# Kernel optimization log

Measured on AMD Instinct MI355X. Metric: run time of the kernel, lower is better.

## Reference

```python
import jax, jax.numpy as jnp
import numpy as np

B = 131072   # batch
D = 128      # input_dim
H = 512      # hidden_dim
E = 2        # number of tasks/experts (fixed in module)
O = 2        # output dim (fixed in module)


def setup_inputs() -> dict:
    key = jax.random.key(0)
    k0, k1, k2, k3 = jax.random.split(key, 4)
    x = jax.random.normal(k0, (B, D), jnp.float32)
    # kaiming-uniform-ish scale for weights
    w1 = jax.random.normal(k1, (E, H, D), jnp.float32) * (1.0 / np.sqrt(D).astype(np.float32))
    b1 = jnp.zeros((E, H), jnp.float32)
    w2 = jax.random.normal(k2, (E, O, H), jnp.float32) * (1.0 / np.sqrt(H).astype(np.float32))
    b2 = jnp.zeros((E, O), jnp.float32)
    # buffer is zeros in torch; randomize so routing is non-degenerate
    prototypes = jax.random.normal(k3, (E, D), jnp.float32)
    return {"x": x, "w1": w1, "b1": b1, "w2": w2, "b2": b2, "prototypes": prototypes}


def reference(x, w1, b1, w2, b2, prototypes):
    # Routing: torch.cdist -> argmin. Squared distance has the same argmin
    # as euclidean distance (sqrt is monotone), so skip the sqrt.
    diff = x[:, None, :] - prototypes[None, :, :]          # [B, E, D]
    d2 = jnp.sum(diff * diff, axis=-1)                     # [B, E]
    t = jnp.argmin(d2, axis=1)                             # [B] int

    # Only E=2 experts: evaluate both and select, instead of a per-sample
    # gathered [B,H,D] weight tensor (this replaces the torch python loop).
    h = jax.nn.relu(jnp.einsum('bd,ehd->beh', x, w1) + b1[None])   # [B, E, H]
    out_all = jnp.einsum('beh,eoh->beo', h, w2) + b2[None]          # [B, E, O]
    out = jnp.take_along_axis(out_all, t[:, None, None], axis=1)[:, 0, :]  # [B, O]
    return out
```

## Files before the change

kernel.cpp:

```cpp
#include <hip/hip_runtime.h>

typedef __bf16 bf16x8 __attribute__((ext_vector_type(8)));
typedef float floatx4 __attribute__((ext_vector_type(4)));

#define XS 136

__device__ __forceinline__ unsigned short f32_bf16(float f) {
    union { float f; unsigned int u; } c; c.f = f;
    return (unsigned short)((c.u + 0x7fffu + ((c.u >> 16) & 1u)) >> 16);
}

__global__ __launch_bounds__(256) void prep_w1_frag(const float* __restrict__ w1,
                                                    unsigned short* __restrict__ wbf) {
    int g    = blockIdx.x * 256 + threadIdx.x;
    int lane = g & 63;
    int frag = g >> 6;
    int ks   = frag & 3;
    int nt   = (frag >> 2) & 31;
    int e    = frag >> 7;
    int l15  = lane & 15;
    int quad = lane >> 4;
    int h    = l15 * 32 + nt;
    const float* src = w1 + ((e * 512 + h) * 128 + ks * 32 + quad * 8);
    unsigned short* dst = wbf + (long)g * 8;
    #pragma unroll
    for (int j = 0; j < 8; ++j) dst[j] = f32_bf16(src[j]);
}

__global__ __launch_bounds__(256, 2) void moe_fused(
    const float* __restrict__ x,
    const unsigned short* __restrict__ wbf,
    const float* __restrict__ b1,
    const float* __restrict__ w2,
    const float* __restrict__ b2,
    const float* __restrict__ protos,
    float* __restrict__ out)
{
    __shared__ unsigned short xs[128 * XS];
    __shared__ float out_s[2][128][2][2];
    __shared__ int   t_s[128];

    const int tid   = threadIdx.x;
    const int lane  = tid & 63;
    const int wave  = tid >> 6;
    const int quad  = lane >> 4;
    const int l15   = lane & 15;
    const int slice = wave & 1;
    const int e     = wave >> 1;
    const long rowbase = (long)blockIdx.x * 128;

    {
        int r   = tid >> 1;
        int sub = tid & 1;
        const float* xr = x + (rowbase + r) * 128 + sub * 64;
        const float* p0 = protos + sub * 64;
        const float* p1 = protos + 128 + sub * 64;
        double acc = 0.0;
        #pragma unroll
        for (int k = 0; k < 16; ++k) {
            float4 xv = *(const float4*)(xr + k * 4);
            float4 a  = *(const float4*)(p0 + k * 4);
            float4 b  = *(const float4*)(p1 + k * 4);
            acc += ((double)a.x - b.x) * (0.5 * ((double)a.x + b.x) - xv.x);
            acc += ((double)a.y - b.y) * (0.5 * ((double)a.y + b.y) - xv.y);
            acc += ((double)a.z - b.z) * (0.5 * ((double)a.z + b.z) - xv.z);
            acc += ((double)a.w - b.w) * (0.5 * ((double)a.w + b.w) - xv.w);
        }
        acc += __shfl_xor(acc, 1);
        if (sub == 0) t_s[r] = (acc > 0.0) ? 1 : 0;
    }

    for (int i = tid; i < 128 * 32; i += 256) {
        int r  = i >> 5;
        int c4 = (i & 31) * 4;
        float4 v = *(const float4*)(x + (rowbase + r) * 128 + c4);
        ushort4 p;
        p.x = f32_bf16(v.x); p.y = f32_bf16(v.y);
        p.z = f32_bf16(v.z); p.w = f32_bf16(v.w);
        *(ushort4*)&xs[r * XS + c4] = p;
    }
    __syncthreads();

    bf16x8 afrag[8][4];
    #pragma unroll
    for (int mt = 0; mt < 8; ++mt) {
        int r = mt * 16 + l15;
        #pragma unroll
        for (int ks = 0; ks < 4; ++ks)
            afrag[mt][ks] = *(const bf16x8*)&xs[r * XS + ks * 32 + quad * 8];
    }

    float outp[8][4][2] = {};

    const bf16x8* wb8 = (const bf16x8*)wbf + (long)((e * 32 + slice * 16) * 4) * 64 + lane;
    const int    coff = e * 512 + l15 * 32 + slice * 16;
    const float* b1p  = b1 + coff;
    const float* w2ap = w2 + e * 1024 + l15 * 32 + slice * 16;
    const float* w2bp = w2ap + 512;
    for (int nt = 0; nt < 16; ++nt) {
        const bf16x8* wp = wb8 + nt * 256;
        bf16x8 bf0 = wp[0];
        bf16x8 bf1 = wp[64];
        bf16x8 bf2 = wp[128];
        bf16x8 bf3 = wp[192];
        float bb  = b1p[nt];
        float w2a = w2ap[nt];
        float w2b = w2bp[nt];
        #pragma unroll
        for (int mt = 0; mt < 8; ++mt) {
            floatx4 c = {bb, bb, bb, bb};
            c = __builtin_amdgcn_mfma_f32_16x16x32_bf16(afrag[mt][0], bf0, c, 0, 0, 0);
            c = __builtin_amdgcn_mfma_f32_16x16x32_bf16(afrag[mt][1], bf1, c, 0, 0, 0);
            c = __builtin_amdgcn_mfma_f32_16x16x32_bf16(afrag[mt][2], bf2, c, 0, 0, 0);
            c = __builtin_amdgcn_mfma_f32_16x16x32_bf16(afrag[mt][3], bf3, c, 0, 0, 0);
            #pragma unroll
            for (int rg = 0; rg < 4; ++rg) {
                float h = fmaxf(c[rg], 0.0f);
                outp[mt][rg][0] = fmaf(h, w2a, outp[mt][rg][0]);
                outp[mt][rg][1] = fmaf(h, w2b, outp[mt][rg][1]);
            }
        }
    }

    #pragma unroll
    for (int mt = 0; mt < 8; ++mt)
        #pragma unroll
        for (int rg = 0; rg < 4; ++rg) {
            float v0 = outp[mt][rg][0];
            float v1 = outp[mt][rg][1];
            v0 += __shfl_xor(v0, 1);  v1 += __shfl_xor(v1, 1);
            v0 += __shfl_xor(v0, 2);  v1 += __shfl_xor(v1, 2);
            v0 += __shfl_xor(v0, 4);  v1 += __shfl_xor(v1, 4);
            v0 += __shfl_xor(v0, 8);  v1 += __shfl_xor(v1, 8);
            if (l15 == 0) {
                int r = mt * 16 + quad * 4 + rg;
                out_s[slice][r][e][0] = v0;
                out_s[slice][r][e][1] = v1;
            }
        }
    __syncthreads();

    {
        int r  = tid >> 1;
        int o  = tid & 1;
        int te = t_s[r];
        out[(rowbase + r) * 2 + o] =
            out_s[0][r][te][o] + out_s[1][r][te][o] + b2[te * 2 + o];
    }
}

extern "C" void kernel_launch(void* const* d_in, const int* in_sizes, int n_in,
                              void* d_out, int out_size, void* d_ws, size_t ws_size,
                              hipStream_t stream) {
    const float* x      = (const float*)d_in[0];
    const float* w1     = (const float*)d_in[1];
    const float* b1     = (const float*)d_in[2];
    const float* w2     = (const float*)d_in[3];
    const float* b2     = (const float*)d_in[4];
    const float* protos = (const float*)d_in[5];
    float* out = (float*)d_out;
    unsigned short* wbf = (unsigned short*)d_ws;

    prep_w1_frag<<<dim3(64), dim3(256), 0, stream>>>(w1, wbf);
    moe_fused<<<dim3(1024), dim3(256), 0, stream>>>(x, wbf, b1, w2, b2, protos, out);
}
```

Before: 158.3 us.

## Split waves over row halves, prefetch weight fragments, and loop persistent tiles

Each wave now covers half of the 128 rows (64) across the full hidden dimension of its expert, where before it covered all rows over half the hidden dimension. This halves the A-fragment registers and removes the cross-slice reduction through shared memory. The hidden-tile loop software-prefetches the next bf16 weight fragments, bias and w2 values, and the kernel launches 512 blocks that each process two row tiles. Occupancy is raised to 3 blocks per SIMD. In exchange, each wave now reads the full weight set for its expert (double the per-wave weight loads), and the extra syncs in the tile loop can serialise the x load with compute.

```diff
diff --git a/kernel.cpp b/kernel.cpp
--- a/kernel.cpp
+++ b/kernel.cpp
@@ -27,7 +27,7 @@
     for (int j = 0; j < 8; ++j) dst[j] = f32_bf16(src[j]);
 }
 
-__global__ __launch_bounds__(256, 2) void moe_fused(
+__global__ __launch_bounds__(256, 3) void moe_fused(
     const float* __restrict__ x,
     const unsigned short* __restrict__ wbf,
     const float* __restrict__ b1,
@@ -37,115 +37,118 @@
     float* __restrict__ out)
 {
     __shared__ unsigned short xs[128 * XS];
-    __shared__ float out_s[2][128][2][2];
+    __shared__ float out_s[128][2][2];
     __shared__ int   t_s[128];
 
-    const int tid   = threadIdx.x;
-    const int lane  = tid & 63;
-    const int wave  = tid >> 6;
-    const int quad  = lane >> 4;
-    const int l15   = lane & 15;
-    const int slice = wave & 1;
-    const int e     = wave >> 1;
-    const long rowbase = (long)blockIdx.x * 128;
+    const int tid  = threadIdx.x;
+    const int lane = tid & 63;
+    const int wave = tid >> 6;
+    const int quad = lane >> 4;
+    const int l15  = lane & 15;
+    const int mh   = wave & 1;
+    const int e    = wave >> 1;
 
-    {
-        int r   = tid >> 1;
-        int sub = tid & 1;
-        const float* xr = x + (rowbase + r) * 128 + sub * 64;
-        const float* p0 = protos + sub * 64;
-        const float* p1 = protos + 128 + sub * 64;
-        double acc = 0.0;
+    for (int tile = blockIdx.x; tile < 1024; tile += 512) {
+        const long rowbase = (long)tile * 128;
+        __syncthreads();
+
+        {
+            int r   = tid >> 1;
+            int sub = tid & 1;
+            const float* xr = x + (rowbase + r) * 128 + sub * 64;
+            const float* p0 = protos + sub * 64;
+            const float* p1 = protos + 128 + sub * 64;
+            double acc = 0.0;
+            #pragma unroll
+            for (int k = 0; k < 16; ++k) {
+                float4 xv = *(const float4*)(xr + k * 4);
+                float4 a  = *(const float4*)(p0 + k * 4);
+                float4 b  = *(const float4*)(p1 + k * 4);
+                acc += ((double)a.x - b.x) * (0.5 * ((double)a.x + b.x) - xv.x);
+                acc += ((double)a.y - b.y) * (0.5 * ((double)a.y + b.y) - xv.y);
+                acc += ((double)a.z - b.z) * (0.5 * ((double)a.z + b.z) - xv.z);
+                acc += ((double)a.w - b.w) * (0.5 * ((double)a.w + b.w) - xv.w);
+            }
+            acc += __shfl_xor(acc, 1);
+            if (sub == 0) t_s[r] = (acc > 0.0) ? 1 : 0;
+        }
+
+        for (int i = tid; i < 128 * 32; i += 256) {
+            int r  = i >> 5;
+            int c4 = (i & 31) * 4;
+            float4 v = *(const float4*)(x + (rowbase + r) * 128 + c4);
+            ushort4 p;
+            p.x = f32_bf16(v.x); p.y = f32_bf16(v.y);
+            p.z = f32_bf16(v.z); p.w = f32_bf16(v.w);
+            *(ushort4*)&xs[r * XS + c4] = p;
+        }
+        __syncthreads();
+
+        bf16x8 afrag[4][4];
         #pragma unroll
-        for (int k = 0; k < 16; ++k) {
-            float4 xv = *(const float4*)(xr + k * 4);
-            float4 a  = *(const float4*)(p0 + k * 4);
-            float4 b  = *(const float4*)(p1 + k * 4);
-            acc += ((double)a.x - b.x) * (0.5 * ((double)a.x + b.x) - xv.x);
-            acc += ((double)a.y - b.y) * (0.5 * ((double)a.y + b.y) - xv.y);
-            acc += ((double)a.z - b.z) * (0.5 * ((double)a.z + b.z) - xv.z);
-            acc += ((double)a.w - b.w) * (0.5 * ((double)a.w + b.w) - xv.w);
+        for (int mt = 0; mt < 4; ++mt) {
+            int r = mh * 64 + mt * 16 + l15;
+            #pragma unroll
+            for (int ks = 0; ks < 4; ++ks)
+                afrag[mt][ks] = *(const bf16x8*)&xs[r * XS + ks * 32 + quad * 8];
         }
-        acc += __shfl_xor(acc, 1);
-        if (sub == 0) t_s[r] = (acc > 0.0) ? 1 : 0;
-    }
 
-    for (int i = tid; i < 128 * 32; i += 256) {
-        int r  = i >> 5;
-        int c4 = (i & 31) * 4;
-        float4 v = *(const float4*)(x + (rowbase + r) * 128 + c4);
-        ushort4 p;
-        p.x = f32_bf16(v.x); p.y = f32_bf16(v.y);
-        p.z = f32_bf16(v.z); p.w = f32_bf16(v.w);
-        *(ushort4*)&xs[r * XS + c4] = p;
-    }
-    __syncthreads();
+        float outp[4][4][2] = {};
 
-    bf16x8 afrag[8][4];
-    #pragma unroll
-    for (int mt = 0; mt < 8; ++mt) {
-        int r = mt * 16 + l15;
+        const bf16x8* wb8 = (const bf16x8*)wbf + (long)(e * 128) * 64 + lane;
+        const float*  b1p  = b1 + e * 512 + l15 * 32;
+        const float*  w2ap = w2 + e * 1024 + l15 * 32;
+        const float*  w2bp = w2ap + 512;
+        bf16x8 cb0 = wb8[0], cb1 = wb8[64], cb2 = wb8[128], cb3 = wb8[192];
+        float bb = b1p[0], wa = w2ap[0], wc = w2bp[0];
+        #pragma unroll 2
+        for (int nt = 0; nt < 32; ++nt) {
+            int ntn = (nt + 1) & 31;
+            const bf16x8* np_ = wb8 + ntn * 256;
+            bf16x8 nb0 = np_[0], nb1 = np_[64], nb2 = np_[128], nb3 = np_[192];
+            float nbb = b1p[ntn], nwa = w2ap[ntn], nwc = w2bp[ntn];
+            #pragma unroll
+            for (int mt = 0; mt < 4; ++mt) {
+                floatx4 c = {bb, bb, bb, bb};
+                c = __builtin_amdgcn_mfma_f32_16x16x32_bf16(afrag[mt][0], cb0, c, 0, 0, 0);
+                c = __builtin_amdgcn_mfma_f32_16x16x32_bf16(afrag[mt][1], cb1, c, 0, 0, 0);
+                c = __builtin_amdgcn_mfma_f32_16x16x32_bf16(afrag[mt][2], cb2, c, 0, 0, 0);
+                c = __builtin_amdgcn_mfma_f32_16x16x32_bf16(afrag[mt][3], cb3, c, 0, 0, 0);
+                #pragma unroll
+                for (int rg = 0; rg < 4; ++rg) {
+                    float h = fmaxf(c[rg], 0.0f);
+                    outp[mt][rg][0] = fmaf(h, wa, outp[mt][rg][0]);
+                    outp[mt][rg][1] = fmaf(h, wc, outp[mt][rg][1]);
+                }
+            }
+            cb0 = nb0; cb1 = nb1; cb2 = nb2; cb3 = nb3;
+            bb = nbb; wa = nwa; wc = nwc;
+        }
+
         #pragma unroll
-        for (int ks = 0; ks < 4; ++ks)
-            afrag[mt][ks] = *(const bf16x8*)&xs[r * XS + ks * 32 + quad * 8];
-    }
-
-    float outp[8][4][2] = {};
-
-    const bf16x8* wb8 = (const bf16x8*)wbf + (long)((e * 32 + slice * 16) * 4) * 64 + lane;
-    const int    coff = e * 512 + l15 * 32 + slice * 16;
-    const float* b1p  = b1 + coff;
-    const float* w2ap = w2 + e * 1024 + l15 * 32 + slice * 16;
-    const float* w2bp = w2ap + 512;
-    for (int nt = 0; nt < 16; ++nt) {
-        const bf16x8* wp = wb8 + nt * 256;
-        bf16x8 bf0 = wp[0];
-        bf16x8 bf1 = wp[64];
-        bf16x8 bf2 = wp[128];
-        bf16x8 bf3 = wp[192];
-        float bb  = b1p[nt];
-        float w2a = w2ap[nt];
-        float w2b = w2bp[nt];
-        #pragma unroll
-        for (int mt = 0; mt < 8; ++mt) {
-            floatx4 c = {bb, bb, bb, bb};
-            c = __builtin_amdgcn_mfma_f32_16x16x32_bf16(afrag[mt][0], bf0, c, 0, 0, 0);
-            c = __builtin_amdgcn_mfma_f32_16x16x32_bf16(afrag[mt][1], bf1, c, 0, 0, 0);
-            c = __builtin_amdgcn_mfma_f32_16x16x32_bf16(afrag[mt][2], bf2, c, 0, 0, 0);
-            c = __builtin_amdgcn_mfma_f32_16x16x32_bf16(afrag[mt][3], bf3, c, 0, 0, 0);
+        for (int mt = 0; mt < 4; ++mt)
             #pragma unroll
             for (int rg = 0; rg < 4; ++rg) {
-                float h = fmaxf(c[rg], 0.0f);
-                outp[mt][rg][0] = fmaf(h, w2a, outp[mt][rg][0]);
-                outp[mt][rg][1] = fmaf(h, w2b, outp[mt][rg][1]);
+                float v0 = outp[mt][rg][0];
+                float v1 = outp[mt][rg][1];
+                v0 += __shfl_xor(v0, 1);  v1 += __shfl_xor(v1, 1);
+                v0 += __shfl_xor(v0, 2);  v1 += __shfl_xor(v1, 2);
+                v0 += __shfl_xor(v0, 4);  v1 += __shfl_xor(v1, 4);
+                v0 += __shfl_xor(v0, 8);  v1 += __shfl_xor(v1, 8);
+                if (l15 == 0) {
+                    int r = mh * 64 + mt * 16 + quad * 4 + rg;
+                    out_s[r][e][0] = v0;
+                    out_s[r][e][1] = v1;
+                }
             }
+        __syncthreads();
+
+        {
+            int r  = tid >> 1;
+            int o  = tid & 1;
+            int te = t_s[r];
+            out[(rowbase + r) * 2 + o] = out_s[r][te][o] + b2[te * 2 + o];
         }
-    }
-
-    #pragma unroll
-    for (int mt = 0; mt < 8; ++mt)
-        #pragma unroll
-        for (int rg = 0; rg < 4; ++rg) {
-            float v0 = outp[mt][rg][0];
-            float v1 = outp[mt][rg][1];
-            v0 += __shfl_xor(v0, 1);  v1 += __shfl_xor(v1, 1);
-            v0 += __shfl_xor(v0, 2);  v1 += __shfl_xor(v1, 2);
-            v0 += __shfl_xor(v0, 4);  v1 += __shfl_xor(v1, 4);
-            v0 += __shfl_xor(v0, 8);  v1 += __shfl_xor(v1, 8);
-            if (l15 == 0) {
-                int r = mt * 16 + quad * 4 + rg;
-                out_s[slice][r][e][0] = v0;
-                out_s[slice][r][e][1] = v1;
-            }
-        }
-    __syncthreads();
-
-    {
-        int r  = tid >> 1;
-        int o  = tid & 1;
-        int te = t_s[r];
-        out[(rowbase + r) * 2 + o] =
-            out_s[0][r][te][o] + out_s[1][r][te][o] + b2[te * 2 + o];
     }
 }
 
@@ -162,5 +165,5 @@
     unsigned short* wbf = (unsigned short*)d_ws;
 
     prep_w1_frag<<<dim3(64), dim3(256), 0, stream>>>(w1, wbf);
-    moe_fused<<<dim3(1024), dim3(256), 0, stream>>>(x, wbf, b1, w2, b2, protos, out);
+    moe_fused<<<dim3(512), dim3(256), 0, stream>>>(x, wbf, b1, w2, b2, protos, out);
 }
```

Measured after the change: 286.7 us. 81.1% more time.
